# Kernel optimization log

Hardware: AMD Instinct MI355X
Metric: run time of the kernel (lower is better)

The kernel has to match this reference:

```python
import jax, jax.numpy as jnp
import numpy as np

STATE_DIM = 1024
INPUT_DIM = 256
OUTPUT_DIM = 256
KX = 10
LAM = 5.0
BSZ = 16
SEQ = 2048


def setup_inputs() -> dict:
    key = jax.random.key(0)
    ks = jax.random.split(key, 6)
    inputs = jax.random.normal(ks[0], (BSZ, SEQ, INPUT_DIM), dtype=jnp.float32)
    h0 = jax.random.normal(ks[1], (STATE_DIM,), dtype=jnp.float32)
    # exponential_decay_init: entries in (exp(-lam), 1)
    A = jnp.exp(-LAM * jax.random.uniform(ks[2], (STATE_DIM,), dtype=jnp.float32))
    B = jax.random.normal(ks[3], (INPUT_DIM, STATE_DIM), dtype=jnp.float32) / INPUT_DIM
    C = jax.random.normal(ks[4], (STATE_DIM, OUTPUT_DIM), dtype=jnp.float32) / STATE_DIM
    M = jax.random.normal(ks[5], (OUTPUT_DIM, INPUT_DIM, KX), dtype=jnp.float32) / OUTPUT_DIM
    return {"inputs": inputs, "h0": h0, "A": A, "B": B, "C": C, "M": M}


def _lds_forward(inputs, h0, A, B, C, M):
    bsz, L, _ = inputs.shape
    S = A.shape[0]
    kx = M.shape[-1]
    # input projection: u_t @ B  -> [B, L, S]
    uB = jnp.einsum('bld,ds->bls', inputs, B)
    # diagonal linear recurrence h_t = A * h_{t-1} + uB_t, h_{-1} = h0,
    # via parallel associative scan on affine maps (a, b): h -> a*h + b
    a = jnp.broadcast_to(A, (1, L, S))

    def combine(x, y):
        a1, b1 = x
        a2, b2 = y
        return (a1 * a2, a2 * b1 + b2)

    Pa, Pb = jax.lax.associative_scan(combine, (a, uB), axis=1)
    all_h = Pa * h0 + Pb                              # [B, L, S]
    lds_out = jnp.einsum('bls,so->blo', all_h, C)      # [B, L, O]
    # shift forward by kx: new[:, :-kx] = lds_out[:, kx:], tail zeros
    new_lds = jnp.pad(lds_out[:, kx:, :], ((0, 0), (0, kx), (0, 0)))
    # AR term: ar[b,t,o] = sum_{i<kx} M[o,:,i] . x[b, t-i, :] (zero-padded past)
    ar = jnp.zeros_like(new_lds)
    for i in range(kx):
        x_i = jnp.pad(inputs, ((0, 0), (i, 0), (0, 0)))[:, :L, :]
        ar = ar + jnp.einsum('oj,blj->blo', M[:, :, i], x_i)
    return ar + new_lds


def reference(inputs, h0, A, B, C, M):
    return _lds_forward(inputs, h0, A, B, C, M)
```

## Files before the change

### kernel.cpp

```cpp
#include <hip/hip_runtime.h>

#define BSZn 16
#define SEQn 2048
#define DIN 256
#define DST 1024
#define DOUTn 256
#define KXn 10
#define TCH 64
#define NCH 32
#define ROWSB 2064

typedef __attribute__((ext_vector_type(4))) float f32x4;
typedef __attribute__((ext_vector_type(8))) short bf16x8;

__device__ __forceinline__ unsigned short f2bf(float f){
  unsigned u = __float_as_uint(f);
  u += 0x7FFF + ((u>>16)&1);
  return (unsigned short)(u>>16);
}
__device__ __forceinline__ float bf2f(unsigned short s){
  return __uint_as_float(((unsigned)s)<<16);
}

#define XIDX(r,c) ((((r)<<8) + (c)) ^ (((r)&7)<<3))

__global__ void k_prep(const float* __restrict__ B, const float* __restrict__ C,
                       const float* __restrict__ M, unsigned short* __restrict__ Bt2,
                       unsigned short* __restrict__ Ct2, unsigned short* __restrict__ Mt2){
  int stride = gridDim.x*blockDim.x;
  int i0 = blockIdx.x*blockDim.x + threadIdx.x;
  for(int idx=i0; idx<DIN*DST; idx+=stride){
    int kb = idx>>15, s = (idx>>5)&1023, dl = idx&31;
    int d = (kb<<5)+dl;
    Bt2[idx] = f2bf(B[d*DST + s]);
  }
  for(int idx=i0; idx<DST*DOUTn; idx+=stride){
    int kb = idx>>13, o = (idx>>5)&255, sl = idx&31;
    int s = (kb<<5)+sl;
    Ct2[idx] = f2bf(C[s*DOUTn + o]);
  }
  for(int idx=i0; idx<DOUTn*DIN*KXn; idx+=stride){
    int kq = idx>>13, o = (idx>>5)&255, kl = idx&31;
    int k = (kq<<5)+kl, ii = k>>8, j = k&255;
    Mt2[idx] = f2bf(M[(o*DIN+j)*KXn + ii]);
  }
}

__global__ __launch_bounds__(256) void k_ub(const float* __restrict__ x,
    const unsigned short* __restrict__ Bt2, const float* __restrict__ A,
    unsigned short* __restrict__ uB, float* __restrict__ P){
  __shared__ __align__(16) unsigned short xt[64*256];
  int wg = blockIdx.x;
  int q = wg & 3, c = (wg>>2)&31, b = wg>>7;
  int t0 = c*TCH, s0 = q<<8;
  const float* xb = x + (size_t)b*SEQn*DIN;
  int tid = threadIdx.x;
  for(int e = tid; e < 64*64; e += 256){
    int r = e>>6, c4 = (e&63)<<2;
    float4 v = *(const float4*)(xb + (t0+r)*DIN + c4);
    ushort4 w; w.x=f2bf(v.x); w.y=f2bf(v.y); w.z=f2bf(v.z); w.w=f2bf(v.w);
    *(ushort4*)&xt[XIDX(r,c4)] = w;
  }
  __syncthreads();
  int wv = tid>>6, ln = tid&63, lm = ln&15, lk = (ln>>4)<<3, rr = (ln>>4)<<2;
  f32x4 zf = {0.f,0.f,0.f,0.f};
  f32x4 acc[4][4];
  #pragma unroll
  for(int tt=0;tt<4;tt++)
    #pragma unroll
    for(int nt=0;nt<4;nt++) acc[tt][nt] = zf;
  #pragma unroll
  for(int kb=0;kb<8;kb++){
    bf16x8 af[4];
    #pragma unroll
    for(int tt=0;tt<4;tt++)
      af[tt] = *(const bf16x8*)&xt[XIDX((tt<<4)+lm, (kb<<5)+lk)];
    #pragma unroll
    for(int nt=0;nt<4;nt++){
      int sg = s0 + (wv<<6) + (nt<<4) + lm;
      bf16x8 bfr = *(const bf16x8*)&Bt2[(kb<<15) + (sg<<5) + lk];
      #pragma unroll
      for(int tt=0;tt<4;tt++)
        acc[tt][nt] = __builtin_amdgcn_mfma_f32_16x16x32_bf16(af[tt], bfr, acc[tt][nt], 0,0,0);
    }
  }
  __syncthreads();
  #pragma unroll
  for(int tt=0;tt<4;tt++)
    #pragma unroll
    for(int nt=0;nt<4;nt++)
      #pragma unroll
      for(int r4=0;r4<4;r4++)
        xt[XIDX((tt<<4)+rr+r4, (wv<<6)+(nt<<4)+lm)] = f2bf(acc[tt][nt][r4]);
  __syncthreads();
  unsigned short* uBp = uB + ((size_t)b*ROWSB + t0)*DST + s0;
  #pragma unroll
  for(int it=0; it<8; it++){
    int j = it*256 + tid;
    int r = j>>5, c0 = (j&31)<<3;
    bf16x8 v = *(const bf16x8*)&xt[XIDX(r,c0)];
    *(bf16x8*)&uBp[(size_t)r*DST + c0] = v;
  }
  {
    int s = s0 + tid;
    float Av = A[s];
    float p = 0.f;
    #pragma unroll
    for(int t=0;t<64;t++)
      p = fmaf(Av, p, bf2f(xt[XIDX(t, tid)]));
    P[(((b<<5)+c)<<10) + s] = p;
  }
}

__global__ void k_bound(const float* __restrict__ A, const float* __restrict__ h0,
                        const float* __restrict__ P, float* __restrict__ bound){
  int i = blockIdx.x*blockDim.x + threadIdx.x;
  if(i >= BSZn*DST) return;
  int b = i >> 10, s = i & 1023;
  float Av = A[s];
  float a2=Av*Av, a4=a2*a2, a8=a4*a4, a16=a8*a8, a32=a16*a16, a64=a32*a32;
  const float* Pb = P + ((size_t)(b<<5)<<10);
  float* Bb = bound + ((size_t)(b<<5)<<10);
  float h = h0[s];
  Bb[s] = h;
  for(int c=1;c<NCH;c++){
    h = fmaf(a64, h, Pb[((c-1)<<10)+s]);
    Bb[(c<<10)+s] = h;
  }
}

__global__ __launch_bounds__(256) void k_h(unsigned short* __restrict__ uB,
    const float* __restrict__ A, const float* __restrict__ bound){
  int wg = blockIdx.x;
  int c = wg & 31, b = wg >> 5;
  int tid = threadIdx.x;
  int s = tid << 2;
  float Av[4], h[4];
  const float* bp = bound + (((size_t)(b<<5)+c)<<10) + s;
  #pragma unroll
  for(int j=0;j<4;j++){ Av[j] = A[s+j]; h[j] = bp[j]; }
  unsigned short* base = uB + ((size_t)b*ROWSB + c*TCH)*DST;
  int kb = s>>5, sl = s&31;
  for(int T=0; T<4; T++){
    unsigned v[16][2];
    #pragma unroll
    for(int r=0;r<16;r++){
      const unsigned* p = (const unsigned*)(base + (size_t)(T*16+r)*DST + s);
      v[r][0] = p[0]; v[r][1] = p[1];
    }
    __syncthreads();
    #pragma unroll
    for(int r=0;r<16;r++){
      float u0 = bf2f((unsigned short)(v[r][0]&0xffff)), u1 = bf2f((unsigned short)(v[r][0]>>16));
      float u2 = bf2f((unsigned short)(v[r][1]&0xffff)), u3 = bf2f((unsigned short)(v[r][1]>>16));
      h[0] = fmaf(Av[0],h[0],u0); h[1] = fmaf(Av[1],h[1],u1);
      h[2] = fmaf(Av[2],h[2],u2); h[3] = fmaf(Av[3],h[3],u3);
      v[r][0] = (unsigned)f2bf(h[0]) | (((unsigned)f2bf(h[1]))<<16);
      v[r][1] = (unsigned)f2bf(h[2]) | (((unsigned)f2bf(h[3]))<<16);
    }
    unsigned* wp = (unsigned*)(uB + (((size_t)b*129 + c*4 + T)*32 + kb)*512 + sl);
    #pragma unroll
    for(int r=0;r<16;r++){
      wp[r*16]   = v[r][0];
      wp[r*16+1] = v[r][1];
    }
    __syncthreads();
  }
  if(c == 31){
    unsigned* zp = (unsigned*)(uB + (((size_t)b*129 + 128)*32)*512);
    for(int e = tid; e < 8192; e += 256) zp[e] = 0u;
  }
}

__global__ __launch_bounds__(256) void k_arc(const float* __restrict__ x,
    const unsigned short* __restrict__ Mt2, const unsigned short* __restrict__ Ct2,
    const unsigned short* __restrict__ h2, float* __restrict__ out){
  __shared__ __align__(16) unsigned short xt[73*256];
  int wg = blockIdx.x;
  int b = wg>>5, c = wg&31;
  int t0 = c*TCH;
  const float* xb = x + (size_t)b*SEQn*DIN;
  int tid = threadIdx.x;
  for(int e = tid; e < 73*64; e += 256){
    int r = e>>6, c4 = (e&63)<<2;
    int t = t0 - 9 + r;
    float4 v = {0.f,0.f,0.f,0.f};
    if(t >= 0) v = *(const float4*)(xb + t*DIN + c4);
    ushort4 w; w.x=f2bf(v.x); w.y=f2bf(v.y); w.z=f2bf(v.z); w.w=f2bf(v.w);
    *(ushort4*)&xt[XIDX(r, c4)] = w;
  }
  __syncthreads();
  int wv = tid>>6, ln = tid&63, lm = ln&15, lk = (ln>>4)<<3, rr = (ln>>4)<<2;
  f32x4 zf = {0.f,0.f,0.f,0.f};
  f32x4 acc[4][4];
  #pragma unroll
  for(int tt=0;tt<4;tt++)
    #pragma unroll
    for(int nt=0;nt<4;nt++) acc[tt][nt] = zf;
  for(int i=0;i<KXn;i++){
    #pragma unroll
    for(int kb8=0;kb8<8;kb8++){
      int col = (kb8<<5) + lk;
      int kq = i*8 + kb8;
      bf16x8 af[4];
      #pragma unroll
      for(int tt=0;tt<4;tt++)
        af[tt] = *(const bf16x8*)&xt[XIDX((tt<<4)+lm + 9 - i, col)];
      #pragma unroll
      for(int nt=0;nt<4;nt++){
        int o = (wv<<6) + (nt<<4) + lm;
        bf16x8 bfr = *(const bf16x8*)&Mt2[(kq<<13) + (o<<5) + lk];
        #pragma unroll
        for(int tt=0;tt<4;tt++)
          acc[tt][nt] = __builtin_amdgcn_mfma_f32_16x16x32_bf16(af[tt], bfr, acc[tt][nt], 0,0,0);
      }
    }
  }
  const unsigned short* hb = h2 + (size_t)b*129*32*512;
  int Tg0 = c*4 + (lm>=6 ? 1 : 0);
  int rowin = (lm<6) ? (10+lm) : (lm-6);
  for(int kb=0;kb<32;kb++){
    bf16x8 af[4];
    #pragma unroll
    for(int tt=0;tt<4;tt++)
      af[tt] = *(const bf16x8*)&hb[(((size_t)(Tg0+tt))*32 + kb)*512 + rowin*32 + lk];
    #pragma unroll
    for(int nt=0;nt<4;nt++){
      int o = (wv<<6) + (nt<<4) + lm;
      bf16x8 bfr = *(const bf16x8*)&Ct2[(kb<<13) + (o<<5) + lk];
      #pragma unroll
      for(int tt=0;tt<4;tt++)
        acc[tt][nt] = __builtin_amdgcn_mfma_f32_16x16x32_bf16(af[tt], bfr, acc[tt][nt], 0,0,0);
    }
  }
  #pragma unroll
  for(int tt=0;tt<4;tt++)
    #pragma unroll
    for(int nt=0;nt<4;nt++)
      #pragma unroll
      for(int r4=0;r4<4;r4++){
        int m = (tt<<4) + rr + r4;
        int o = (wv<<6) + (nt<<4) + lm;
        out[((size_t)b*SEQn + t0 + m)*DOUTn + o] = acc[tt][nt][r4];
      }
}

extern "C" void kernel_launch(void* const* d_in, const int* in_sizes, int n_in,
                              void* d_out, int out_size, void* d_ws, size_t ws_size,
                              hipStream_t stream){
  const float* x  = (const float*)d_in[0];
  const float* h0 = (const float*)d_in[1];
  const float* A  = (const float*)d_in[2];
  const float* B  = (const float*)d_in[3];
  const float* C  = (const float*)d_in[4];
  const float* M  = (const float*)d_in[5];
  float* out = (float*)d_out;
  unsigned short* Bt2 = (unsigned short*)d_ws;
  unsigned short* Ct2 = Bt2 + DIN*DST;
  unsigned short* Mt2 = Ct2 + DST*DOUTn;
  float* P     = (float*)((char*)d_ws + ( 4u<<20));
  float* bound = (float*)((char*)d_ws + ( 6u<<20));
  unsigned short* uB = (unsigned short*)((char*)d_ws + (8u<<20));
  k_prep <<<512, 256, 0, stream>>>(B, C, M, Bt2, Ct2, Mt2);
  k_ub   <<<BSZn*NCH*4, 256, 0, stream>>>(x, Bt2, A, uB, P);
  k_bound<<<(BSZn*DST)/256, 256, 0, stream>>>(A, h0, P, bound);
  k_h    <<<BSZn*NCH, 256, 0, stream>>>(uB, A, bound);
  k_arc  <<<BSZn*NCH, 256, 0, stream>>>(x, Mt2, Ct2, uB, out);
}
```

Baseline: 238.4 us.

## Write uB directly in tiled layout, scan in place, split output across blocks

k_ub now writes the projected inputs straight into the blocked [chunk][kb][row][32] layout that k_arc reads, and zeroes the padding tile itself, so k_h no longer has to remap rows. k_h becomes an in-place per-column scan over two state elements per thread, with twice as many blocks. k_arc splits the output columns into two halves per block, doubling the grid, and sets a launch bound of 4 blocks per SM to raise occupancy. In exchange, the x tile load in k_arc is repeated per half, and k_h's strided 4-byte accesses may coalesce less well.

```diff
diff --git a/kernel.cpp b/kernel.cpp
--- a/kernel.cpp
+++ b/kernel.cpp
@@ -8,7 +8,6 @@
 #define KXn 10
 #define TCH 64
 #define NCH 32
-#define ROWSB 2064
 
 typedef __attribute__((ext_vector_type(4))) float f32x4;
 typedef __attribute__((ext_vector_type(8))) short bf16x8;
@@ -23,6 +22,7 @@
 }
 
 #define XIDX(r,c) ((((r)<<8) + (c)) ^ (((r)&7)<<3))
+
 
 __global__ void k_prep(const float* __restrict__ B, const float* __restrict__ C,
                        const float* __restrict__ M, unsigned short* __restrict__ Bt2,
@@ -93,13 +93,19 @@
       for(int r4=0;r4<4;r4++)
         xt[XIDX((tt<<4)+rr+r4, (wv<<6)+(nt<<4)+lm)] = f2bf(acc[tt][nt][r4]);
   __syncthreads();
-  unsigned short* uBp = uB + ((size_t)b*ROWSB + t0)*DST + s0;
+  unsigned short* hb = uB + ((size_t)b*129)*32*512;
   #pragma unroll
   for(int it=0; it<8; it++){
     int j = it*256 + tid;
     int r = j>>5, c0 = (j&31)<<3;
     bf16x8 v = *(const bf16x8*)&xt[XIDX(r,c0)];
-    *(bf16x8*)&uBp[(size_t)r*DST + c0] = v;
+    int s = s0 + c0;
+    size_t addr = (((size_t)(c*4 + (r>>4)))*32 + (s>>5))*512 + ((r&15)<<5) + (s&31);
+    *(bf16x8*)&hb[addr] = v;
+  }
+  if(c == 31){
+    unsigned* zp = (unsigned*)(uB + (((size_t)b*129 + 128)*32 + (q<<3))*512);
+    for(int e = tid; e < 2048; e += 256) zp[e] = 0u;
   }
   {
     int s = s0 + tid;
@@ -132,52 +138,29 @@
 __global__ __launch_bounds__(256) void k_h(unsigned short* __restrict__ uB,
     const float* __restrict__ A, const float* __restrict__ bound){
   int wg = blockIdx.x;
-  int c = wg & 31, b = wg >> 5;
+  int half = wg & 1, c = (wg>>1) & 31, b = wg >> 6;
   int tid = threadIdx.x;
-  int s = tid << 2;
-  float Av[4], h[4];
+  int s = (half<<9) + (tid<<1);
+  float Av0 = A[s], Av1 = A[s+1];
   const float* bp = bound + (((size_t)(b<<5)+c)<<10) + s;
-  #pragma unroll
-  for(int j=0;j<4;j++){ Av[j] = A[s+j]; h[j] = bp[j]; }
-  unsigned short* base = uB + ((size_t)b*ROWSB + c*TCH)*DST;
-  int kb = s>>5, sl = s&31;
-  for(int T=0; T<4; T++){
-    unsigned v[16][2];
-    #pragma unroll
-    for(int r=0;r<16;r++){
-      const unsigned* p = (const unsigned*)(base + (size_t)(T*16+r)*DST + s);
-      v[r][0] = p[0]; v[r][1] = p[1];
-    }
-    __syncthreads();
-    #pragma unroll
-    for(int r=0;r<16;r++){
-      float u0 = bf2f((unsigned short)(v[r][0]&0xffff)), u1 = bf2f((unsigned short)(v[r][0]>>16));
-      float u2 = bf2f((unsigned short)(v[r][1]&0xffff)), u3 = bf2f((unsigned short)(v[r][1]>>16));
-      h[0] = fmaf(Av[0],h[0],u0); h[1] = fmaf(Av[1],h[1],u1);
-      h[2] = fmaf(Av[2],h[2],u2); h[3] = fmaf(Av[3],h[3],u3);
-      v[r][0] = (unsigned)f2bf(h[0]) | (((unsigned)f2bf(h[1]))<<16);
-      v[r][1] = (unsigned)f2bf(h[2]) | (((unsigned)f2bf(h[3]))<<16);
-    }
-    unsigned* wp = (unsigned*)(uB + (((size_t)b*129 + c*4 + T)*32 + kb)*512 + sl);
-    #pragma unroll
-    for(int r=0;r<16;r++){
-      wp[r*16]   = v[r][0];
-      wp[r*16+1] = v[r][1];
-    }
-    __syncthreads();
-  }
-  if(c == 31){
-    unsigned* zp = (unsigned*)(uB + (((size_t)b*129 + 128)*32)*512);
-    for(int e = tid; e < 8192; e += 256) zp[e] = 0u;
-  }
-}
-
-__global__ __launch_bounds__(256) void k_arc(const float* __restrict__ x,
+  float h0v = bp[0], h1v = bp[1];
+  unsigned short* hb = uB + (((size_t)b*129 + c*4)*32 + (s>>5))*512 + (s&31);
+  #pragma unroll 4
+  for(int t=0;t<64;t++){
+    unsigned* p = (unsigned*)(hb + ((t>>4)*32*512) + ((t&15)<<5));
+    unsigned v = *p;
+    h0v = fmaf(Av0, h0v, bf2f((unsigned short)(v & 0xffff)));
+    h1v = fmaf(Av1, h1v, bf2f((unsigned short)(v >> 16)));
+    *p = (unsigned)f2bf(h0v) | (((unsigned)f2bf(h1v))<<16);
+  }
+}
+
+__global__ __launch_bounds__(256,4) void k_arc(const float* __restrict__ x,
     const unsigned short* __restrict__ Mt2, const unsigned short* __restrict__ Ct2,
     const unsigned short* __restrict__ h2, float* __restrict__ out){
   __shared__ __align__(16) unsigned short xt[73*256];
   int wg = blockIdx.x;
-  int b = wg>>5, c = wg&31;
+  int oh = wg & 1, c = (wg>>1)&31, b = wg>>6;
   int t0 = c*TCH;
   const float* xb = x + (size_t)b*SEQn*DIN;
   int tid = threadIdx.x;
@@ -191,12 +174,13 @@
   }
   __syncthreads();
   int wv = tid>>6, ln = tid&63, lm = ln&15, lk = (ln>>4)<<3, rr = (ln>>4)<<2;
+  int obase = (oh<<7) + (wv<<5);
   f32x4 zf = {0.f,0.f,0.f,0.f};
-  f32x4 acc[4][4];
-  #pragma unroll
-  for(int tt=0;tt<4;tt++)
-    #pragma unroll
-    for(int nt=0;nt<4;nt++) acc[tt][nt] = zf;
+  f32x4 acc[4][2];
+  #pragma unroll
+  for(int tt=0;tt<4;tt++)
+    #pragma unroll
+    for(int nt=0;nt<2;nt++) acc[tt][nt] = zf;
   for(int i=0;i<KXn;i++){
     #pragma unroll
     for(int kb8=0;kb8<8;kb8++){
@@ -207,8 +191,8 @@
       for(int tt=0;tt<4;tt++)
         af[tt] = *(const bf16x8*)&xt[XIDX((tt<<4)+lm + 9 - i, col)];
       #pragma unroll
-      for(int nt=0;nt<4;nt++){
-        int o = (wv<<6) + (nt<<4) + lm;
+      for(int nt=0;nt<2;nt++){
+        int o = obase + (nt<<4) + lm;
         bf16x8 bfr = *(const bf16x8*)&Mt2[(kq<<13) + (o<<5) + lk];
         #pragma unroll
         for(int tt=0;tt<4;tt++)
@@ -219,14 +203,15 @@
   const unsigned short* hb = h2 + (size_t)b*129*32*512;
   int Tg0 = c*4 + (lm>=6 ? 1 : 0);
   int rowin = (lm<6) ? (10+lm) : (lm-6);
+  #pragma unroll
   for(int kb=0;kb<32;kb++){
     bf16x8 af[4];
     #pragma unroll
     for(int tt=0;tt<4;tt++)
       af[tt] = *(const bf16x8*)&hb[(((size_t)(Tg0+tt))*32 + kb)*512 + rowin*32 + lk];
     #pragma unroll
-    for(int nt=0;nt<4;nt++){
-      int o = (wv<<6) + (nt<<4) + lm;
+    for(int nt=0;nt<2;nt++){
+      int o = obase + (nt<<4) + lm;
       bf16x8 bfr = *(const bf16x8*)&Ct2[(kb<<13) + (o<<5) + lk];
       #pragma unroll
       for(int tt=0;tt<4;tt++)
@@ -236,11 +221,11 @@
   #pragma unroll
   for(int tt=0;tt<4;tt++)
     #pragma unroll
-    for(int nt=0;nt<4;nt++)
+    for(int nt=0;nt<2;nt++)
       #pragma unroll
       for(int r4=0;r4<4;r4++){
         int m = (tt<<4) + rr + r4;
-        int o = (wv<<6) + (nt<<4) + lm;
+        int o = obase + (nt<<4) + lm;
         out[((size_t)b*SEQn + t0 + m)*DOUTn + o] = acc[tt][nt][r4];
       }
 }
@@ -264,6 +249,6 @@
   k_prep <<<512, 256, 0, stream>>>(B, C, M, Bt2, Ct2, Mt2);
   k_ub   <<<BSZn*NCH*4, 256, 0, stream>>>(x, Bt2, A, uB, P);
   k_bound<<<(BSZn*DST)/256, 256, 0, stream>>>(A, h0, P, bound);
-  k_h    <<<BSZn*NCH, 256, 0, stream>>>(uB, A, bound);
-  k_arc  <<<BSZn*NCH, 256, 0, stream>>>(x, Mt2, Ct2, uB, out);
-}
+  k_h    <<<BSZn*NCH*2, 256, 0, stream>>>(uB, A, bound);
+  k_arc  <<<BSZn*NCH*2, 256, 0, stream>>>(x, Mt2, Ct2, uB, out);
+}
```

After: 276.8 us. 1.16x slower.
